# Optimization experiments

Hardware: AMD Instinct MI355X
Metric: run time of the kernel (lower is better)

The kernel has to match this reference:

```python
import jax, jax.numpy as jnp
import numpy as np

B, T, D, R = 4, 2048, 1024, 64  # batch, seq_len, hidden_dim, max_relative_position


def setup_inputs() -> dict:
    key = jax.random.key(0)
    ks = jax.random.split(key, 11)
    s = 1.0 / np.sqrt(D)

    def lin(k):
        return (jax.random.normal(k, (D, D), jnp.float32) * s)

    return {
        "repre": jax.random.normal(ks[0], (B, T, D), jnp.float32),
        "mask": jnp.ones((B, T, T), jnp.int32),  # 1 = valid position
        "st_Wq": lin(ks[1]), "st_bq": jnp.zeros((D,), jnp.float32),
        "st_Wk": lin(ks[2]), "st_bk": jnp.zeros((D,), jnp.float32),
        "st_rel": jax.random.normal(ks[3], (2 * R + 1, D), jnp.float32) * 0.02,
        "ed_Wq": lin(ks[4]), "ed_bq": jnp.zeros((D,), jnp.float32),
        "ed_Wk": lin(ks[5]), "ed_bk": jnp.zeros((D,), jnp.float32),
        "ed_rel": jax.random.normal(ks[6], (2 * R + 1, D), jnp.float32) * 0.02,
    }


def _attn_logits(x, Wq, bq, Wk, bk, rel, mask):
    # Single-head attention scores with relative-position key bias (OpenNMT style).
    d = x.shape[-1]
    q = (x @ Wq + bq) * (1.0 / jnp.sqrt(jnp.float32(d)))  # [B,T,D], pre-scaled query
    k = x @ Wk + bk                                        # [B,T,D]
    scores = jnp.einsum('btd,bsd->bts', q, k)              # [B,T,T] content scores
    Tn = x.shape[1]
    Rn = (rel.shape[0] - 1) // 2
    pos = jnp.arange(Tn)
    # relative position matrix: clip(j - i, -R, R) + R  -> [T,T] indices
    idx = jnp.clip(pos[None, :] - pos[:, None], -Rn, Rn) + Rn
    # q . rel_emb for every relative offset, then gather per (i,j):
    # equivalent to einsum('btd,tsd->bts', q, rel[idx]) without the [T,T,D] gather.
    qr = jnp.einsum('btd,rd->btr', q, rel)                 # [B,T,2R+1]
    scores = scores + qr[:, pos[:, None], idx]             # [B,T,T]
    return jnp.where(mask.astype(bool), scores, jnp.float32(-1e18))


def reference(repre, mask, st_Wq, st_bq, st_Wk, st_bk, st_rel,
              ed_Wq, ed_bq, ed_Wk, ed_bk, ed_rel):
    span_st_logits = _attn_logits(repre, st_Wq, st_bq, st_Wk, st_bk, st_rel, mask)
    span_ed_logits = _attn_logits(repre, ed_Wq, ed_bq, ed_Wk, ed_bk, ed_rel, mask)
    return (span_st_logits, span_ed_logits)
```

## Files before the change

kernel.cpp:

```cpp
#include <hip/hip_runtime.h>

constexpr int Bn = 4;
constexpr int Tn = 2048;
constexpr int Dn = 1024;
constexpr int Rn = 64;
constexpr int RELP = 256;
constexpr int QR_STRIDE = 132;

typedef __bf16 bf8 __attribute__((ext_vector_type(8)));
typedef float f32x4 __attribute__((ext_vector_type(4)));

__device__ __forceinline__ unsigned short f2bf(float f) {
    unsigned int u = __float_as_uint(f);
    u += 0x7fffu + ((u >> 16) & 1u);
    return (unsigned short)(u >> 16);
}

#define GLDS(g, l)                                                            \
    __builtin_amdgcn_global_load_lds(                                         \
        (const __attribute__((address_space(1))) void*)(g),                   \
        (__attribute__((address_space(3))) void*)(l), 16, 0, 0)

__device__ __forceinline__ void mfma_gemm_128(
    const unsigned short* __restrict__ Ab,
    const unsigned short* __restrict__ Bb,
    int K, f32x4 acc[4][4],
    unsigned short* As, unsigned short* Bs)
{
    const int tid = threadIdx.x;
    const int r0  = tid >> 2;
    const int c8  = (tid & 3) * 8;
    const int lane = tid & 63;
    const int w    = tid >> 6;
    const int wm = (w & 1) * 64, wn = (w >> 1) * 64;
    const int l15 = lane & 15, lq = lane >> 4;

    for (int k0 = 0; k0 < K; k0 += 32) {
        __syncthreads();
        GLDS(Ab + (size_t)r0 * K + k0 + c8,        As + r0 * 32 + c8);
        GLDS(Ab + ((size_t)r0 + 64) * K + k0 + c8, As + (r0 + 64) * 32 + c8);
        GLDS(Bb + (size_t)r0 * K + k0 + c8,        Bs + r0 * 32 + c8);
        GLDS(Bb + ((size_t)r0 + 64) * K + k0 + c8, Bs + (r0 + 64) * 32 + c8);
        __syncthreads();
        bf8 a[4], b[4];
#pragma unroll
        for (int i = 0; i < 4; ++i) {
            a[i] = *(const bf8*)&As[(wm + i * 16 + l15) * 32 + lq * 8];
            b[i] = *(const bf8*)&Bs[(wn + i * 16 + l15) * 32 + lq * 8];
        }
#pragma unroll
        for (int i = 0; i < 4; ++i)
#pragma unroll
            for (int j = 0; j < 4; ++j)
                acc[i][j] = __builtin_amdgcn_mfma_f32_16x16x32_bf16(
                    a[i], b[j], acc[i][j], 0, 0, 0);
    }
}

__global__ __launch_bounds__(256) void cvt_bf16(
    const float* __restrict__ in, unsigned short* __restrict__ out, int n4)
{
    int i = blockIdx.x * 256 + threadIdx.x;
    if (i < n4) {
        float4 v = ((const float4*)in)[i];
        ushort4 o;
        o.x = f2bf(v.x); o.y = f2bf(v.y); o.z = f2bf(v.z); o.w = f2bf(v.w);
        ((ushort4*)out)[i] = o;
    }
}

__global__ __launch_bounds__(256) void wt_transpose(
    const float* __restrict__ w0, const float* __restrict__ w1,
    const float* __restrict__ w2, const float* __restrict__ w3,
    unsigned short* __restrict__ WT)
{
    __shared__ float t[32][33];
    const int z = blockIdx.z;
    const float* W = z == 0 ? w0 : z == 1 ? w1 : z == 2 ? w2 : w3;
    const int x = blockIdx.x * 32 + threadIdx.x;
    const int y0 = blockIdx.y * 32;
#pragma unroll
    for (int j = 0; j < 32; j += 8)
        t[threadIdx.y + j][threadIdx.x] = W[(size_t)(y0 + threadIdx.y + j) * Dn + x];
    __syncthreads();
    unsigned short* o = WT + (size_t)z * Dn * Dn;
    const int n0 = blockIdx.x * 32;
#pragma unroll
    for (int j = 0; j < 32; j += 8)
        o[(size_t)(n0 + threadIdx.y + j) * Dn + y0 + threadIdx.x] =
            f2bf(t[threadIdx.x][threadIdx.y + j]);
}

__global__ __launch_bounds__(256) void rel_pad(
    const float* __restrict__ st_rel, const float* __restrict__ ed_rel,
    unsigned short* __restrict__ relb)
{
    const int z = blockIdx.y;
    const float* in = z ? ed_rel : st_rel;
    const int i4 = blockIdx.x * 256 + threadIdx.x;
    const int row = (i4 * 4) >> 10;
    const int col = (i4 * 4) & 1023;
    ushort4 o; o.x = 0; o.y = 0; o.z = 0; o.w = 0;
    if (row < 2 * Rn + 1) {
        float4 v = *(const float4*)(in + (size_t)row * 1024 + col);
        o.x = f2bf(v.x); o.y = f2bf(v.y); o.z = f2bf(v.z); o.w = f2bf(v.w);
    }
    ((ushort4*)(relb + (size_t)z * RELP * 1024))[i4] = o;
}

__global__ __launch_bounds__(256) void proj_gemm(
    const unsigned short* __restrict__ Xb, const unsigned short* __restrict__ Wb,
    const float* __restrict__ b0, const float* __restrict__ b1,
    const float* __restrict__ b2, const float* __restrict__ b3,
    unsigned short* __restrict__ outQK, float qscale)
{
    __shared__ unsigned short As[128 * 32], Bs[128 * 32];
    const int z = blockIdx.z;
    const float* bias = z == 0 ? b0 : z == 1 ? b1 : z == 2 ? b2 : b3;
    const float scale = (z & 1) ? 1.0f : qscale;

    const unsigned short* Ab = Xb + (size_t)blockIdx.x * 128 * Dn;
    const unsigned short* Bb = Wb + ((size_t)z * Dn + blockIdx.y * 128) * Dn;

    f32x4 zero = {0.f, 0.f, 0.f, 0.f};
    f32x4 acc[4][4];
#pragma unroll
    for (int i = 0; i < 4; ++i)
#pragma unroll
        for (int j = 0; j < 4; ++j) acc[i][j] = zero;

    mfma_gemm_128(Ab, Bb, Dn, acc, As, Bs);

    const int tid = threadIdx.x, lane = tid & 63, w = tid >> 6;
    const int wm = (w & 1) * 64, wn = (w >> 1) * 64;
    const int l15 = lane & 15, lq = lane >> 4;
    unsigned short* out = outQK + (size_t)z * (size_t)Bn * Tn * Dn;

#pragma unroll
    for (int ni = 0; ni < 4; ++ni) {
        const int col = blockIdx.y * 128 + wn + ni * 16 + l15;
        const float bv = bias[col];
#pragma unroll
        for (int mi = 0; mi < 4; ++mi) {
#pragma unroll
            for (int r = 0; r < 4; ++r) {
                const int row = blockIdx.x * 128 + wm + mi * 16 + lq * 4 + r;
                out[(size_t)row * Dn + col] = f2bf((acc[mi][ni][r] + bv) * scale);
            }
        }
    }
}

__global__ __launch_bounds__(256) void qr_gemm(
    const unsigned short* __restrict__ QKb, const unsigned short* __restrict__ relb,
    float* __restrict__ QR)
{
    __shared__ unsigned short As[128 * 32], Bs[128 * 32];
    const int z = blockIdx.z;
    const unsigned short* Ab = QKb + ((size_t)(z * 2) * Bn * Tn + blockIdx.x * 128) * Dn;
    const unsigned short* Bb = relb + ((size_t)z * RELP + blockIdx.y * 128) * Dn;

    f32x4 zero = {0.f, 0.f, 0.f, 0.f};
    f32x4 acc[4][4];
#pragma unroll
    for (int i = 0; i < 4; ++i)
#pragma unroll
        for (int j = 0; j < 4; ++j) acc[i][j] = zero;

    mfma_gemm_128(Ab, Bb, Dn, acc, As, Bs);

    const int tid = threadIdx.x, lane = tid & 63, w = tid >> 6;
    const int wm = (w & 1) * 64, wn = (w >> 1) * 64;
    const int l15 = lane & 15, lq = lane >> 4;
    float* out = QR + (size_t)z * (size_t)Bn * Tn * QR_STRIDE;

#pragma unroll
    for (int ni = 0; ni < 4; ++ni) {
        const int col = blockIdx.y * 128 + wn + ni * 16 + l15;
        if (col >= 2 * Rn + 1) continue;
#pragma unroll
        for (int mi = 0; mi < 4; ++mi) {
#pragma unroll
            for (int r = 0; r < 4; ++r) {
                const int row = blockIdx.x * 128 + wm + mi * 16 + lq * 4 + r;
                out[(size_t)row * QR_STRIDE + col] = acc[mi][ni][r];
            }
        }
    }
}

__global__ __launch_bounds__(256) void scores_gemm(
    const unsigned short* __restrict__ QKb, const float* __restrict__ QR,
    const int* __restrict__ mask, float* __restrict__ Out)
{
    __shared__ unsigned short As[128 * 32], Bs[128 * 32];
    const int z = blockIdx.z;
    const int side = z >> 2, bt = z & 3;

    const unsigned short* Ab =
        QKb + ((size_t)side * 2 * Bn * Tn + (size_t)bt * Tn + blockIdx.x * 128) * Dn;
    const unsigned short* Bb =
        QKb + (((size_t)side * 2 + 1) * Bn * Tn + (size_t)bt * Tn + blockIdx.y * 128) * Dn;
    const float* QRb = QR + ((size_t)side * Bn * Tn + (size_t)bt * Tn) * QR_STRIDE;
    const int* maskb = mask + (size_t)bt * Tn * Tn;
    float* outb = Out + ((size_t)side * Bn + bt) * (size_t)Tn * Tn;

    f32x4 zero = {0.f, 0.f, 0.f, 0.f};
    f32x4 acc[4][4];
#pragma unroll
    for (int i = 0; i < 4; ++i)
#pragma unroll
        for (int j = 0; j < 4; ++j) acc[i][j] = zero;

    mfma_gemm_128(Ab, Bb, Dn, acc, As, Bs);

    const int tid = threadIdx.x, lane = tid & 63, w = tid >> 6;
    const int wm = (w & 1) * 64, wn = (w >> 1) * 64;
    const int l15 = lane & 15, lq = lane >> 4;

#pragma unroll
    for (int mi = 0; mi < 4; ++mi) {
#pragma unroll
        for (int r = 0; r < 4; ++r) {
            const int i = blockIdx.x * 128 + wm + mi * 16 + lq * 4 + r;
            const float* qrow = QRb + (size_t)i * QR_STRIDE;
            const int* mrow = maskb + (size_t)i * Tn;
            float* orow = outb + (size_t)i * Tn;
#pragma unroll
            for (int ni = 0; ni < 4; ++ni) {
                const int j = blockIdx.y * 128 + wn + ni * 16 + l15;
                int d = j - i;
                d = d < -Rn ? -Rn : (d > Rn ? Rn : d);
                const float qv = qrow[d + Rn];
                orow[j] = mrow[j] ? acc[mi][ni][r] + qv : -1e18f;
            }
        }
    }
}

extern "C" void kernel_launch(void* const* d_in, const int* in_sizes, int n_in,
                              void* d_out, int out_size, void* d_ws, size_t ws_size,
                              hipStream_t stream) {
    const float* repre  = (const float*)d_in[0];
    const int*   mask   = (const int*)  d_in[1];
    const float* st_Wq  = (const float*)d_in[2];
    const float* st_bq  = (const float*)d_in[3];
    const float* st_Wk  = (const float*)d_in[4];
    const float* st_bk  = (const float*)d_in[5];
    const float* st_rel = (const float*)d_in[6];
    const float* ed_Wq  = (const float*)d_in[7];
    const float* ed_bq  = (const float*)d_in[8];
    const float* ed_Wk  = (const float*)d_in[9];
    const float* ed_bk  = (const float*)d_in[10];
    const float* ed_rel = (const float*)d_in[11];
    float* out = (float*)d_out;

    const size_t MT = (size_t)Bn * Tn;

    unsigned short* Xb   = (unsigned short*)d_ws;
    unsigned short* Wb   = Xb + MT * Dn;
    unsigned short* relb = Wb + (size_t)4 * Dn * Dn;
    unsigned short* QKb  = relb + (size_t)2 * RELP * Dn;
    float* QRbuf = (float*)(QKb + (size_t)4 * MT * Dn);

    const float qscale = 0.03125f;
    dim3 blk(256);

    {
        int n4 = (int)(MT * Dn / 4);
        cvt_bf16<<<dim3((n4 + 255) / 256), blk, 0, stream>>>(repre, Xb, n4);
        wt_transpose<<<dim3(32, 32, 4), dim3(32, 8), 0, stream>>>(
            st_Wq, st_Wk, ed_Wq, ed_Wk, Wb);
        rel_pad<<<dim3(RELP * Dn / 4 / 256, 2), blk, 0, stream>>>(st_rel, ed_rel, relb);
    }

    proj_gemm<<<dim3((int)MT / 128, Dn / 128, 4), blk, 0, stream>>>(
        Xb, Wb, st_bq, st_bk, ed_bq, ed_bk, QKb, qscale);

    qr_gemm<<<dim3((int)MT / 128, RELP / 128, 2), blk, 0, stream>>>(QKb, relb, QRbuf);

    scores_gemm<<<dim3(Tn / 128, Tn / 128, 8), blk, 0, stream>>>(QKb, QRbuf, mask, out);
}
```

Baseline: 533.1 us.

## Double-buffer GEMM LDS tiles with register-staged global prefetch

Replaces the direct global-to-LDS loads with register-staged prefetching into a double-buffered LDS tile. The next K-slice's global loads are issued before the MFMA loop and written to the other buffer afterwards, leaving one barrier per iteration instead of two. The goal is to hide global memory latency behind MFMA work, at the cost of doubled LDS per block (possibly lower occupancy) and more VGPRs for the staging registers.

```diff
diff --git a/kernel.cpp b/kernel.cpp
--- a/kernel.cpp
+++ b/kernel.cpp
@@ -15,11 +15,6 @@
     u += 0x7fffu + ((u >> 16) & 1u);
     return (unsigned short)(u >> 16);
 }
-
-#define GLDS(g, l)                                                            \
-    __builtin_amdgcn_global_load_lds(                                         \
-        (const __attribute__((address_space(1))) void*)(g),                   \
-        (__attribute__((address_space(3))) void*)(l), 16, 0, 0)
 
 __device__ __forceinline__ void mfma_gemm_128(
     const unsigned short* __restrict__ Ab,
@@ -35,18 +30,37 @@
     const int wm = (w & 1) * 64, wn = (w >> 1) * 64;
     const int l15 = lane & 15, lq = lane >> 4;
 
+    const unsigned short* ga0 = Ab + (size_t)r0 * K + c8;
+    const unsigned short* ga1 = Ab + ((size_t)r0 + 64) * K + c8;
+    const unsigned short* gb0 = Bb + (size_t)r0 * K + c8;
+    const unsigned short* gb1 = Bb + ((size_t)r0 + 64) * K + c8;
+
+    int4 ra0 = *(const int4*)(ga0);
+    int4 ra1 = *(const int4*)(ga1);
+    int4 rb0 = *(const int4*)(gb0);
+    int4 rb1 = *(const int4*)(gb1);
+    *(int4*)&As[r0 * 32 + c8]        = ra0;
+    *(int4*)&As[(r0 + 64) * 32 + c8] = ra1;
+    *(int4*)&Bs[r0 * 32 + c8]        = rb0;
+    *(int4*)&Bs[(r0 + 64) * 32 + c8] = rb1;
+
     for (int k0 = 0; k0 < K; k0 += 32) {
+        const int cur = (k0 >> 5) & 1;
         __syncthreads();
-        GLDS(Ab + (size_t)r0 * K + k0 + c8,        As + r0 * 32 + c8);
-        GLDS(Ab + ((size_t)r0 + 64) * K + k0 + c8, As + (r0 + 64) * 32 + c8);
-        GLDS(Bb + (size_t)r0 * K + k0 + c8,        Bs + r0 * 32 + c8);
-        GLDS(Bb + ((size_t)r0 + 64) * K + k0 + c8, Bs + (r0 + 64) * 32 + c8);
-        __syncthreads();
+        const bool more = (k0 + 32) < K;
+        if (more) {
+            ra0 = *(const int4*)(ga0 + k0 + 32);
+            ra1 = *(const int4*)(ga1 + k0 + 32);
+            rb0 = *(const int4*)(gb0 + k0 + 32);
+            rb1 = *(const int4*)(gb1 + k0 + 32);
+        }
+        const unsigned short* Ac = As + cur * (128 * 32);
+        const unsigned short* Bc = Bs + cur * (128 * 32);
         bf8 a[4], b[4];
 #pragma unroll
         for (int i = 0; i < 4; ++i) {
-            a[i] = *(const bf8*)&As[(wm + i * 16 + l15) * 32 + lq * 8];
-            b[i] = *(const bf8*)&Bs[(wn + i * 16 + l15) * 32 + lq * 8];
+            a[i] = *(const bf8*)&Ac[(wm + i * 16 + l15) * 32 + lq * 8];
+            b[i] = *(const bf8*)&Bc[(wn + i * 16 + l15) * 32 + lq * 8];
         }
 #pragma unroll
         for (int i = 0; i < 4; ++i)
@@ -54,6 +68,14 @@
             for (int j = 0; j < 4; ++j)
                 acc[i][j] = __builtin_amdgcn_mfma_f32_16x16x32_bf16(
                     a[i], b[j], acc[i][j], 0, 0, 0);
+        if (more) {
+            unsigned short* An = As + (cur ^ 1) * (128 * 32);
+            unsigned short* Bn = Bs + (cur ^ 1) * (128 * 32);
+            *(int4*)&An[r0 * 32 + c8]        = ra0;
+            *(int4*)&An[(r0 + 64) * 32 + c8] = ra1;
+            *(int4*)&Bn[r0 * 32 + c8]        = rb0;
+            *(int4*)&Bn[(r0 + 64) * 32 + c8] = rb1;
+        }
     }
 }
 
@@ -114,7 +136,7 @@
     const float* __restrict__ b2, const float* __restrict__ b3,
     unsigned short* __restrict__ outQK, float qscale)
 {
-    __shared__ unsigned short As[128 * 32], Bs[128 * 32];
+    __shared__ unsigned short As[2 * 128 * 32], Bs[2 * 128 * 32];
     const int z = blockIdx.z;
     const float* bias = z == 0 ? b0 : z == 1 ? b1 : z == 2 ? b2 : b3;
     const float scale = (z & 1) ? 1.0f : qscale;
@@ -155,7 +177,7 @@
     const unsigned short* __restrict__ QKb, const unsigned short* __restrict__ relb,
     float* __restrict__ QR)
 {
-    __shared__ unsigned short As[128 * 32], Bs[128 * 32];
+    __shared__ unsigned short As[2 * 128 * 32], Bs[2 * 128 * 32];
     const int z = blockIdx.z;
     const unsigned short* Ab = QKb + ((size_t)(z * 2) * Bn * Tn + blockIdx.x * 128) * Dn;
     const unsigned short* Bb = relb + ((size_t)z * RELP + blockIdx.y * 128) * Dn;
@@ -193,7 +215,7 @@
     const unsigned short* __restrict__ QKb, const float* __restrict__ QR,
     const int* __restrict__ mask, float* __restrict__ Out)
 {
-    __shared__ unsigned short As[128 * 32], Bs[128 * 32];
+    __shared__ unsigned short As[2 * 128 * 32], Bs[2 * 128 * 32];
     const int z = blockIdx.z;
     const int side = z >> 2, bt = z & 3;
 
```

Measured after the change: 545.6 us. 1.02x slower.

## Load MFMA fragments directly from global memory, dropping LDS staging and barriers

Applied to the files above, without the earlier changes.

Replaces the shared-memory tiled GEMM core with per-wave direct global loads of bf16 fragments into registers, plus a one-step register double buffer. This removes the LDS staging and the two block barriers per k-iteration. In exchange, the waves sharing a tile duplicate their global reads, and each lane's loads stride across rows, relying on cache hits instead of shared reuse.

```diff
diff --git a/kernel.cpp b/kernel.cpp
--- a/kernel.cpp
+++ b/kernel.cpp
@@ -16,44 +16,49 @@
     return (unsigned short)(u >> 16);
 }
 
-#define GLDS(g, l)                                                            \
-    __builtin_amdgcn_global_load_lds(                                         \
-        (const __attribute__((address_space(1))) void*)(g),                   \
-        (__attribute__((address_space(3))) void*)(l), 16, 0, 0)
-
-__device__ __forceinline__ void mfma_gemm_128(
+template <int K>
+__device__ __forceinline__ void mfma_gemm_direct(
     const unsigned short* __restrict__ Ab,
     const unsigned short* __restrict__ Bb,
-    int K, f32x4 acc[4][4],
-    unsigned short* As, unsigned short* Bs)
+    f32x4 acc[4][4])
 {
     const int tid = threadIdx.x;
-    const int r0  = tid >> 2;
-    const int c8  = (tid & 3) * 8;
-    const int lane = tid & 63;
-    const int w    = tid >> 6;
-    const int wm = (w & 1) * 64, wn = (w >> 1) * 64;
-    const int l15 = lane & 15, lq = lane >> 4;
-
+    const int lane = tid & 63, w = tid >> 6;
+    const int wm = (w & 1) * 64, wn = (w >> 1) * 64;
+    const int l15 = lane & 15, lq = lane >> 4;
+
+    const unsigned short* pa[4];
+    const unsigned short* pb[4];
+#pragma unroll
+    for (int i = 0; i < 4; ++i) {
+        pa[i] = Ab + (size_t)(wm + i * 16 + l15) * K + lq * 8;
+        pb[i] = Bb + (size_t)(wn + i * 16 + l15) * K + lq * 8;
+    }
+
+    bf8 a0[4], b0[4], a1[4], b1[4];
+#pragma unroll
+    for (int i = 0; i < 4; ++i) {
+        a0[i] = *(const bf8*)(pa[i]);
+        b0[i] = *(const bf8*)(pb[i]);
+    }
+
+#pragma unroll 2
     for (int k0 = 0; k0 < K; k0 += 32) {
-        __syncthreads();
-        GLDS(Ab + (size_t)r0 * K + k0 + c8,        As + r0 * 32 + c8);
-        GLDS(Ab + ((size_t)r0 + 64) * K + k0 + c8, As + (r0 + 64) * 32 + c8);
-        GLDS(Bb + (size_t)r0 * K + k0 + c8,        Bs + r0 * 32 + c8);
-        GLDS(Bb + ((size_t)r0 + 64) * K + k0 + c8, Bs + (r0 + 64) * 32 + c8);
-        __syncthreads();
-        bf8 a[4], b[4];
-#pragma unroll
-        for (int i = 0; i < 4; ++i) {
-            a[i] = *(const bf8*)&As[(wm + i * 16 + l15) * 32 + lq * 8];
-            b[i] = *(const bf8*)&Bs[(wn + i * 16 + l15) * 32 + lq * 8];
+        if (k0 + 32 < K) {
+#pragma unroll
+            for (int i = 0; i < 4; ++i) {
+                a1[i] = *(const bf8*)(pa[i] + k0 + 32);
+                b1[i] = *(const bf8*)(pb[i] + k0 + 32);
+            }
         }
 #pragma unroll
         for (int i = 0; i < 4; ++i)
 #pragma unroll
             for (int j = 0; j < 4; ++j)
                 acc[i][j] = __builtin_amdgcn_mfma_f32_16x16x32_bf16(
-                    a[i], b[j], acc[i][j], 0, 0, 0);
+                    a0[i], b0[j], acc[i][j], 0, 0, 0);
+#pragma unroll
+        for (int i = 0; i < 4; ++i) { a0[i] = a1[i]; b0[i] = b1[i]; }
     }
 }
 
@@ -114,7 +119,6 @@
     const float* __restrict__ b2, const float* __restrict__ b3,
     unsigned short* __restrict__ outQK, float qscale)
 {
-    __shared__ unsigned short As[128 * 32], Bs[128 * 32];
     const int z = blockIdx.z;
     const float* bias = z == 0 ? b0 : z == 1 ? b1 : z == 2 ? b2 : b3;
     const float scale = (z & 1) ? 1.0f : qscale;
@@ -129,7 +133,7 @@
 #pragma unroll
         for (int j = 0; j < 4; ++j) acc[i][j] = zero;
 
-    mfma_gemm_128(Ab, Bb, Dn, acc, As, Bs);
+    mfma_gemm_direct<Dn>(Ab, Bb, acc);
 
     const int tid = threadIdx.x, lane = tid & 63, w = tid >> 6;
     const int wm = (w & 1) * 64, wn = (w >> 1) * 64;
@@ -155,7 +159,6 @@
     const unsigned short* __restrict__ QKb, const unsigned short* __restrict__ relb,
     float* __restrict__ QR)
 {
-    __shared__ unsigned short As[128 * 32], Bs[128 * 32];
     const int z = blockIdx.z;
     const unsigned short* Ab = QKb + ((size_t)(z * 2) * Bn * Tn + blockIdx.x * 128) * Dn;
     const unsigned short* Bb = relb + ((size_t)z * RELP + blockIdx.y * 128) * Dn;
@@ -167,7 +170,7 @@
 #pragma unroll
         for (int j = 0; j < 4; ++j) acc[i][j] = zero;
 
-    mfma_gemm_128(Ab, Bb, Dn, acc, As, Bs);
+    mfma_gemm_direct<Dn>(Ab, Bb, acc);
 
     const int tid = threadIdx.x, lane = tid & 63, w = tid >> 6;
     const int wm = (w & 1) * 64, wn = (w >> 1) * 64;
@@ -193,7 +196,6 @@
     const unsigned short* __restrict__ QKb, const float* __restrict__ QR,
     const int* __restrict__ mask, float* __restrict__ Out)
 {
-    __shared__ unsigned short As[128 * 32], Bs[128 * 32];
     const int z = blockIdx.z;
     const int side = z >> 2, bt = z & 3;
 
@@ -212,7 +214,7 @@
 #pragma unroll
         for (int j = 0; j < 4; ++j) acc[i][j] = zero;
 
-    mfma_gemm_128(Ab, Bb, Dn, acc, As, Bs);
+    mfma_gemm_direct<Dn>(Ab, Bb, acc);
 
     const int tid = threadIdx.x, lane = tid & 63, w = tid >> 6;
     const int wm = (w & 1) * 64, wn = (w >> 1) * 64;
```

Measured after the change: 850.9 us. 59.6% more time.
